# Optimization experiments

Hardware: AMD Instinct MI355X
Metric: run time of the kernel (lower is better)

Reference implementation:

```python
import jax, jax.numpy as jnp
import numpy as np

N, K, D = 8192, 128, 512

def setup_inputs() -> dict:
    key = jax.random.key(0)
    kx, kc = jax.random.split(key)
    x = jax.random.normal(kx, (N, D), dtype=jnp.float32)
    centroids = jax.random.normal(kc, (K, D), dtype=jnp.float32)
    return {"x": x, "centroids": centroids}

def reference(x, centroids):
    # Faithful to torch: dist = (x[:,None,:] - centroids[None]).norm(2, dim=2)
    # Broadcast subtract -> [N, K, D] intermediate, then L2 reduction over D.
    diff = x[:, None, :] - centroids[None, :, :]          # [N, K, D]
    dist = jnp.sqrt(jnp.sum(diff * diff, axis=2))         # [N, K]
    return dist
```

## Files before the change

kernel.cpp:

```cpp
#include <hip/hip_runtime.h>
#include <hip/hip_bf16.h>

#define N_ROWS 8192
#define K_CENT 128
#define D_DIM  512
#define LDS_PITCH 520

typedef short v8s __attribute__((ext_vector_type(8)));
typedef unsigned short v8u __attribute__((ext_vector_type(8)));
typedef float v4f __attribute__((ext_vector_type(4)));

__device__ inline unsigned short f2bf(float f) {
    union { float f; unsigned u; } v; v.f = f;
    unsigned r = v.u + 0x7FFFu + ((v.u >> 16) & 1u);
    return (unsigned short)(r >> 16);
}

__global__ __launch_bounds__(256) void prep_centroids(const float* __restrict__ c,
                                                      float* __restrict__ cnorm,
                                                      unsigned short* __restrict__ cb) {
    int wave = (int)((blockIdx.x * blockDim.x + threadIdx.x) >> 6);
    int lane = threadIdx.x & 63;
    if (wave >= K_CENT) return;
    const float* src = c + (size_t)wave * D_DIM;
    float4 a = ((const float4*)src)[lane];
    float4 b = ((const float4*)src)[64 + lane];
    float s = a.x*a.x + a.y*a.y + a.z*a.z + a.w*a.w
            + b.x*b.x + b.y*b.y + b.z*b.z + b.w*b.w;
    #pragma unroll
    for (int off = 32; off >= 1; off >>= 1) s += __shfl_xor(s, off, 64);
    if (lane == 0) cnorm[wave] = s;
    unsigned short* dst = cb + (size_t)wave * D_DIM;
    ushort4 p0, p1;
    p0.x = f2bf(a.x); p0.y = f2bf(a.y); p0.z = f2bf(a.z); p0.w = f2bf(a.w);
    p1.x = f2bf(b.x); p1.y = f2bf(b.y); p1.z = f2bf(b.z); p1.w = f2bf(b.w);
    ((ushort4*)dst)[lane]      = p0;
    ((ushort4*)dst)[64 + lane] = p1;
}

__global__ __launch_bounds__(512, 4) void dist_kernel(const float* __restrict__ x,
                                                      const unsigned short* __restrict__ cb,
                                                      const float* __restrict__ cnorm,
                                                      float* __restrict__ out) {
    __shared__ unsigned short xlds[16 * LDS_PITCH];

    const int t    = threadIdx.x;
    const int lane = t & 63;
    const int g    = t >> 6;
    const int rowbase = blockIdx.x * 16;

    const float* xs = x + (size_t)rowbase * D_DIM;
    #pragma unroll
    for (int j = 0; j < 2; ++j) {
        int base = j * 4096 + t * 8;
        float4 v0 = *(const float4*)(xs + base);
        float4 v1 = *(const float4*)(xs + base + 4);
        int row = base >> 9;
        int k   = base & 511;
        v8u p;
        p[0] = f2bf(v0.x); p[1] = f2bf(v0.y); p[2] = f2bf(v0.z); p[3] = f2bf(v0.w);
        p[4] = f2bf(v1.x); p[5] = f2bf(v1.y); p[6] = f2bf(v1.z); p[7] = f2bf(v1.w);
        *(v8u*)&xlds[row * LDS_PITCH + k] = p;
    }
    __syncthreads();

    const int n16  = lane & 15;
    const int quad = lane >> 4;
    const unsigned short* bptr = cb + (size_t)(g * 16 + n16) * D_DIM + quad * 8;
    const unsigned short* aptr = &xlds[n16 * LDS_PITCH + quad * 8];

    v4f acc  = (v4f){0.f, 0.f, 0.f, 0.f};
    v4f accx = (v4f){0.f, 0.f, 0.f, 0.f};
    #pragma unroll
    for (int i = 0; i < 16; ++i) {
        v8s af = *(const v8s*)(aptr + i * 32);
        v8s bf = *(const v8s*)(bptr + i * 32);
        acc  = __builtin_amdgcn_mfma_f32_16x16x32_bf16(af, bf, acc, 0, 0, 0);
        accx = __builtin_amdgcn_mfma_f32_16x16x32_bf16(af, af, accx, 0, 0, 0);
    }

    const float cn = cnorm[g * 16 + n16];
    #pragma unroll
    for (int r = 0; r < 4; ++r) {
        float xn = __shfl(accx[r], 20 * quad + r, 64);
        int row = rowbase + quad * 4 + r;
        float d2 = xn + cn - 2.0f * acc[r];
        d2 = d2 > 0.f ? d2 : 0.f;
        out[(size_t)row * K_CENT + g * 16 + n16] = sqrtf(d2);
    }
}

__global__ void naive_kernel(const float* __restrict__ x, const float* __restrict__ c,
                             float* __restrict__ out) {
    int idx = blockIdx.x * blockDim.x + threadIdx.x;
    if (idx >= N_ROWS * K_CENT) return;
    int n = idx / K_CENT, k = idx % K_CENT;
    const float* xr = x + (size_t)n * D_DIM;
    const float* cr = c + (size_t)k * D_DIM;
    float s = 0.f;
    for (int d = 0; d < D_DIM; ++d) { float df = xr[d] - cr[d]; s += df * df; }
    out[idx] = sqrtf(s);
}

extern "C" void kernel_launch(void* const* d_in, const int* in_sizes, int n_in,
                              void* d_out, int out_size, void* d_ws, size_t ws_size,
                              hipStream_t stream) {
    const float* x = (const float*)d_in[0];
    const float* c = (const float*)d_in[1];
    float* out = (float*)d_out;

    const size_t need = 512 + (size_t)K_CENT * D_DIM * sizeof(unsigned short);
    if (ws_size < need) {
        int total = N_ROWS * K_CENT;
        naive_kernel<<<(total + 255) / 256, 256, 0, stream>>>(x, c, out);
        return;
    }

    float* cnorm = (float*)d_ws;
    unsigned short* cb = (unsigned short*)((char*)d_ws + 512);

    prep_centroids<<<(K_CENT * 64 + 255) / 256, 256, 0, stream>>>(c, cnorm, cb);
    dist_kernel<<<N_ROWS / 16, 512, 0, stream>>>(x, cb, cnorm, out);
}
```

Baseline: 73.46 us.

## Fuse centroid prep into distance kernel, computing centroid norms via MFMA

```diff
diff --git a/kernel.cpp b/kernel.cpp
--- a/kernel.cpp
+++ b/kernel.cpp
@@ -16,32 +16,9 @@
     return (unsigned short)(r >> 16);
 }
 
-__global__ __launch_bounds__(256) void prep_centroids(const float* __restrict__ c,
-                                                      float* __restrict__ cnorm,
-                                                      unsigned short* __restrict__ cb) {
-    int wave = (int)((blockIdx.x * blockDim.x + threadIdx.x) >> 6);
-    int lane = threadIdx.x & 63;
-    if (wave >= K_CENT) return;
-    const float* src = c + (size_t)wave * D_DIM;
-    float4 a = ((const float4*)src)[lane];
-    float4 b = ((const float4*)src)[64 + lane];
-    float s = a.x*a.x + a.y*a.y + a.z*a.z + a.w*a.w
-            + b.x*b.x + b.y*b.y + b.z*b.z + b.w*b.w;
-    #pragma unroll
-    for (int off = 32; off >= 1; off >>= 1) s += __shfl_xor(s, off, 64);
-    if (lane == 0) cnorm[wave] = s;
-    unsigned short* dst = cb + (size_t)wave * D_DIM;
-    ushort4 p0, p1;
-    p0.x = f2bf(a.x); p0.y = f2bf(a.y); p0.z = f2bf(a.z); p0.w = f2bf(a.w);
-    p1.x = f2bf(b.x); p1.y = f2bf(b.y); p1.z = f2bf(b.z); p1.w = f2bf(b.w);
-    ((ushort4*)dst)[lane]      = p0;
-    ((ushort4*)dst)[64 + lane] = p1;
-}
-
-__global__ __launch_bounds__(512, 4) void dist_kernel(const float* __restrict__ x,
-                                                      const unsigned short* __restrict__ cb,
-                                                      const float* __restrict__ cnorm,
-                                                      float* __restrict__ out) {
+__global__ __launch_bounds__(512, 4) void dist_fused(const float* __restrict__ x,
+                                                     const float* __restrict__ c,
+                                                     float* __restrict__ out) {
     __shared__ unsigned short xlds[16 * LDS_PITCH];
 
     const int t    = threadIdx.x;
@@ -66,20 +43,35 @@
 
     const int n16  = lane & 15;
     const int quad = lane >> 4;
-    const unsigned short* bptr = cb + (size_t)(g * 16 + n16) * D_DIM + quad * 8;
+    const float* cptr = c + (size_t)(g * 16 + n16) * D_DIM + quad * 8;
     const unsigned short* aptr = &xlds[n16 * LDS_PITCH + quad * 8];
 
     v4f acc  = (v4f){0.f, 0.f, 0.f, 0.f};
     v4f accx = (v4f){0.f, 0.f, 0.f, 0.f};
+    v4f accc = (v4f){0.f, 0.f, 0.f, 0.f};
     #pragma unroll
     for (int i = 0; i < 16; ++i) {
+        float4 q0 = *(const float4*)(cptr + i * 32);
+        float4 q1 = *(const float4*)(cptr + i * 32 + 4);
         v8s af = *(const v8s*)(aptr + i * 32);
-        v8s bf = *(const v8s*)(bptr + i * 32);
-        acc  = __builtin_amdgcn_mfma_f32_16x16x32_bf16(af, bf, acc, 0, 0, 0);
+        v8s bf;
+        bf[0] = (short)f2bf(q0.x); bf[1] = (short)f2bf(q0.y);
+        bf[2] = (short)f2bf(q0.z); bf[3] = (short)f2bf(q0.w);
+        bf[4] = (short)f2bf(q1.x); bf[5] = (short)f2bf(q1.y);
+        bf[6] = (short)f2bf(q1.z); bf[7] = (short)f2bf(q1.w);
+        acc  = __builtin_amdgcn_mfma_f32_16x16x32_bf16(af, bf, acc,  0, 0, 0);
         accx = __builtin_amdgcn_mfma_f32_16x16x32_bf16(af, af, accx, 0, 0, 0);
+        accc = __builtin_amdgcn_mfma_f32_16x16x32_bf16(bf, bf, accc, 0, 0, 0);
     }
 
-    const float cn = cnorm[g * 16 + n16];
+    const int csrc = 16 * (n16 >> 2) + n16;
+    float cd0 = __shfl(accc[0], csrc, 64);
+    float cd1 = __shfl(accc[1], csrc, 64);
+    float cd2 = __shfl(accc[2], csrc, 64);
+    float cd3 = __shfl(accc[3], csrc, 64);
+    const int cr = n16 & 3;
+    float cn = cr == 0 ? cd0 : cr == 1 ? cd1 : cr == 2 ? cd2 : cd3;
+
     #pragma unroll
     for (int r = 0; r < 4; ++r) {
         float xn = __shfl(accx[r], 20 * quad + r, 64);
@@ -90,35 +82,13 @@
     }
 }
 
-__global__ void naive_kernel(const float* __restrict__ x, const float* __restrict__ c,
-                             float* __restrict__ out) {
-    int idx = blockIdx.x * blockDim.x + threadIdx.x;
-    if (idx >= N_ROWS * K_CENT) return;
-    int n = idx / K_CENT, k = idx % K_CENT;
-    const float* xr = x + (size_t)n * D_DIM;
-    const float* cr = c + (size_t)k * D_DIM;
-    float s = 0.f;
-    for (int d = 0; d < D_DIM; ++d) { float df = xr[d] - cr[d]; s += df * df; }
-    out[idx] = sqrtf(s);
-}
-
 extern "C" void kernel_launch(void* const* d_in, const int* in_sizes, int n_in,
                               void* d_out, int out_size, void* d_ws, size_t ws_size,
                               hipStream_t stream) {
     const float* x = (const float*)d_in[0];
     const float* c = (const float*)d_in[1];
     float* out = (float*)d_out;
+    (void)d_ws; (void)ws_size;
 
-    const size_t need = 512 + (size_t)K_CENT * D_DIM * sizeof(unsigned short);
-    if (ws_size < need) {
-        int total = N_ROWS * K_CENT;
-        naive_kernel<<<(total + 255) / 256, 256, 0, stream>>>(x, c, out);
-        return;
-    }
-
-    float* cnorm = (float*)d_ws;
-    unsigned short* cb = (unsigned short*)((char*)d_ws + 512);
-
-    prep_centroids<<<(K_CENT * 64 + 255) / 256, 256, 0, stream>>>(c, cnorm, cb);
-    dist_kernel<<<N_ROWS / 16, 512, 0, stream>>>(x, cb, cnorm, out);
+    dist_fused<<<N_ROWS / 16, 512, 0, stream>>>(x, c, out);
 }
```

Measured after the change: 79.10 us. +7.7%, slower.
